# Performance work log

Hardware: AMD Instinct MI355X
Metric: run time of the kernel (lower is better)

Reference implementation:

```python
import jax, jax.numpy as jnp
import numpy as np


def _build_tree(N: int, n: int, seed: int = 0):
    """Random forest encoded as parent pointers + sibling ranks.

    parents:  int32 [N+1]; parents[i] in [0, i) for i>0, root(0) and sentinel(N) -> N.
    child_pos: int32 [N+1]; rank among siblings (in_edges order); >= n means the
               one-hot code is all zeros (matches torch.eye rows beyond n, and roots).
    """
    rng = np.random.default_rng(seed)
    parents = np.empty(N + 1, dtype=np.int32)
    parents[0] = N                      # root -> sentinel
    parents[1:N] = rng.integers(0, np.arange(1, N))  # parent of i is an earlier node
    parents[N] = N                      # sentinel self-loop

    pa = parents[:N].astype(np.int64)
    order = np.argsort(pa, kind="stable")
    sorted_pa = pa[order]
    _, first_idx, inv = np.unique(sorted_pa, return_index=True, return_inverse=True)
    rank = np.arange(N) - first_idx[inv]           # sibling rank within each parent group
    child_pos = np.empty(N + 1, dtype=np.int32)
    child_pos[order] = rank.astype(np.int32)
    child_pos[0] = n                    # root has no parent -> zero code
    child_pos[N] = n                    # sentinel -> zero code
    return parents, child_pos


def setup_inputs() -> dict:
    N, n, k = 262144, 32, 16
    parents, child_pos = _build_tree(N, n)
    return {
        "parents": jnp.asarray(parents),
        "child_pos": jnp.asarray(child_pos),
        "n": n,
        "k": k,
    }


def reference(parents, child_pos, n, k):
    """pos_embeds[node] = concat_{t=0..k-1} onehot(child_pos(ancestor_t(node)), n).

    This is the closed form of the original layer-by-layer scatter:
      pos[child, :n]  = eye row (sibling rank one-hot)
      pos[child, n:]  = pos[parent, :-n]
    Roots keep all-zero codes (child_pos = n -> out-of-range one-hot = zeros).
    """
    N = parents.shape[0] - 1

    def step(cur, _):
        code = jax.nn.one_hot(child_pos[cur], n, dtype=jnp.float32)  # [N, n]
        return parents[cur], code

    _, codes = jax.lax.scan(step, jnp.arange(N, dtype=parents.dtype), None, length=k)
    # codes: [k, N, n] -> [N, k*n] with slot 0 (own code) first
    return jnp.transpose(codes, (1, 0, 2)).reshape(N, k * n)
```

## Files before the change

### kernel.cpp

```cpp
#include <hip/hip_runtime.h>


#define NN 32
#define KK 16

typedef float f32x4 __attribute__((ext_vector_type(4)));

__global__ __launch_bounds__(256) void pe_fused_rl(
    const int* __restrict__ parents,
    const int* __restrict__ child_pos,
    f32x4* __restrict__ out4, int N)
{
    const int lane  = (int)(threadIdx.x & 63);
    const int wid   = (int)((blockIdx.x * blockDim.x + threadIdx.x) >> 6);
    const int wbase = wid * 64;
    const int node  = wbase + lane;

    unsigned int c[4];
    {
        int cur = (node < N) ? node : N;
        #pragma unroll
        for (int w = 0; w < 4; ++w) {
            unsigned int u = 0;
            #pragma unroll
            for (int b = 0; b < 4; ++b) {
                const int cp = child_pos[cur];
                const unsigned int byte = (cp < NN) ? (unsigned int)cp : 0xFFu;
                u |= byte << (8 * b);
                cur = parents[cur];
            }
            c[w] = u;
        }
    }

    const bool hi32 = (lane >= 32);
    const int  sh   = ((lane >> 3) & 3) * 8;
    const int  q4   = (lane & 7) * 4;

    f32x4* wout = out4 + (size_t)wbase * 128 + lane;

    #pragma unroll 4
    for (int r = 0; r < 64; ++r) {
        const unsigned s0 = (unsigned)__builtin_amdgcn_readlane((int)c[0], r);
        const unsigned s1 = (unsigned)__builtin_amdgcn_readlane((int)c[1], r);
        const unsigned s2 = (unsigned)__builtin_amdgcn_readlane((int)c[2], r);
        const unsigned s3 = (unsigned)__builtin_amdgcn_readlane((int)c[3], r);

        const int code0 = (int)(((hi32 ? s1 : s0) >> sh) & 0xFFu);
        const int code1 = (int)(((hi32 ? s3 : s2) >> sh) & 0xFFu);

        f32x4 v0, v1;
        v0.x = (code0 == q4    ) ? 1.0f : 0.0f;
        v0.y = (code0 == q4 + 1) ? 1.0f : 0.0f;
        v0.z = (code0 == q4 + 2) ? 1.0f : 0.0f;
        v0.w = (code0 == q4 + 3) ? 1.0f : 0.0f;
        v1.x = (code1 == q4    ) ? 1.0f : 0.0f;
        v1.y = (code1 == q4 + 1) ? 1.0f : 0.0f;
        v1.z = (code1 == q4 + 2) ? 1.0f : 0.0f;
        v1.w = (code1 == q4 + 3) ? 1.0f : 0.0f;

        wout[(size_t)r * 128]      = v0;
        wout[(size_t)r * 128 + 64] = v1;
    }
}

extern "C" void kernel_launch(void* const* d_in, const int* in_sizes, int n_in,
                              void* d_out, int out_size, void* d_ws, size_t ws_size,
                              hipStream_t stream) {
    const int* parents   = (const int*)d_in[0];
    const int* child_pos = (const int*)d_in[1];
    f32x4* out4 = (f32x4*)d_out;

    const int N = in_sizes[0] - 1;
    const int n_waves = (N + 63) / 64;
    const int grid    = (n_waves + 3) / 4;

    pe_fused_rl<<<grid, 256, 0, stream>>>(parents, child_pos, out4, N);
}
```

Measured before the change: 111.3 us.

## Split ancestor-code gathering and one-hot expansion into two kernels via workspace

The fused kernel becomes two passes. The first kernel walks each node's ancestor chain and writes packed 16-byte codes to the workspace. The second kernel reads those codes, with each wave handling 256 nodes, and streams the one-hot output. The aim is to stop the latency-bound pointer chase from stalling the bandwidth-bound output writes. The cost is an extra launch and a workspace round trip, and the old fused path is kept as a fallback when the workspace is too small.

```diff
diff --git a/kernel.cpp b/kernel.cpp
--- a/kernel.cpp
+++ b/kernel.cpp
@@ -5,6 +5,79 @@
 #define KK 16
 
 typedef float f32x4 __attribute__((ext_vector_type(4)));
+
+__global__ __launch_bounds__(256) void pe_codes(
+    const int* __restrict__ parents,
+    const int* __restrict__ child_pos,
+    uint4* __restrict__ codes_out, int N)
+{
+    const int node = blockIdx.x * blockDim.x + threadIdx.x;
+    if (node >= N) return;
+    unsigned int packed[KK / 4];
+    int cur = node;
+    #pragma unroll
+    for (int w = 0; w < KK / 4; ++w) {
+        unsigned int u = 0;
+        #pragma unroll
+        for (int b = 0; b < 4; ++b) {
+            const int cp = child_pos[cur];
+            const unsigned int byte = (cp < NN) ? (unsigned int)cp : 0xFFu;
+            u |= byte << (8 * b);
+            cur = parents[cur];
+        }
+        packed[w] = u;
+    }
+    codes_out[node] = make_uint4(packed[0], packed[1], packed[2], packed[3]);
+}
+
+__global__ __launch_bounds__(256) void pe_expand_rl(
+    const uint4* __restrict__ codes,
+    f32x4* __restrict__ out4, int N)
+{
+    const int lane  = (int)(threadIdx.x & 63);
+    const int wid   = (int)((blockIdx.x * blockDim.x + threadIdx.x) >> 6);
+    const int wbase = wid * 256;
+
+    uint4 cq[4];
+    #pragma unroll
+    for (int q = 0; q < 4; ++q) {
+        int row = wbase + q * 64 + lane;
+        cq[q] = codes[(row < N) ? row : 0];
+    }
+
+    const bool hi32 = (lane >= 32);
+    const int  sh   = ((lane >> 3) & 3) * 8;
+    const int  q4   = (lane & 7) * 4;
+
+    #pragma unroll
+    for (int q = 0; q < 4; ++q) {
+        if (wbase + q * 64 >= N) break;
+        f32x4* wout = out4 + (size_t)(wbase + q * 64) * 128 + lane;
+        #pragma unroll 4
+        for (int j = 0; j < 64; ++j) {
+            const unsigned s0 = (unsigned)__builtin_amdgcn_readlane((int)cq[q].x, j);
+            const unsigned s1 = (unsigned)__builtin_amdgcn_readlane((int)cq[q].y, j);
+            const unsigned s2 = (unsigned)__builtin_amdgcn_readlane((int)cq[q].z, j);
+            const unsigned s3 = (unsigned)__builtin_amdgcn_readlane((int)cq[q].w, j);
+
+            const int code0 = (int)(((hi32 ? s1 : s0) >> sh) & 0xFFu);
+            const int code1 = (int)(((hi32 ? s3 : s2) >> sh) & 0xFFu);
+
+            f32x4 v0, v1;
+            v0.x = (code0 == q4    ) ? 1.0f : 0.0f;
+            v0.y = (code0 == q4 + 1) ? 1.0f : 0.0f;
+            v0.z = (code0 == q4 + 2) ? 1.0f : 0.0f;
+            v0.w = (code0 == q4 + 3) ? 1.0f : 0.0f;
+            v1.x = (code1 == q4    ) ? 1.0f : 0.0f;
+            v1.y = (code1 == q4 + 1) ? 1.0f : 0.0f;
+            v1.z = (code1 == q4 + 2) ? 1.0f : 0.0f;
+            v1.w = (code1 == q4 + 3) ? 1.0f : 0.0f;
+
+            wout[(size_t)j * 128]      = v0;
+            wout[(size_t)j * 128 + 64] = v1;
+        }
+    }
+}
 
 __global__ __launch_bounds__(256) void pe_fused_rl(
     const int* __restrict__ parents,
@@ -72,8 +145,17 @@
     f32x4* out4 = (f32x4*)d_out;
 
     const int N = in_sizes[0] - 1;
-    const int n_waves = (N + 63) / 64;
-    const int grid    = (n_waves + 3) / 4;
 
-    pe_fused_rl<<<grid, 256, 0, stream>>>(parents, child_pos, out4, N);
+    if (ws_size >= (size_t)N * KK) {
+        pe_codes<<<(N + 255) / 256, 256, 0, stream>>>(
+            parents, child_pos, (uint4*)d_ws, N);
+
+        const int n_waves = (N + 255) / 256;
+        const int grid    = (n_waves + 3) / 4;
+        pe_expand_rl<<<grid, 256, 0, stream>>>((const uint4*)d_ws, out4, N);
+    } else {
+        const int n_waves = (N + 63) / 64;
+        const int grid    = (n_waves + 3) / 4;
+        pe_fused_rl<<<grid, 256, 0, stream>>>(parents, child_pos, out4, N);
+    }
 }
```

New measurement: 122.2 us. 9.8% more time.
